# Optimization experiments

Hardware: AMD Instinct MI355X
Metric: run time of the kernel (lower is better)

Reference implementation:

```python
import jax, jax.numpy as jnp
import numpy as np

H, LMAX, NSEG, EPS = 8, 2, 16, 1e-7
S = (LMAX + 1) ** 2  # 9 spherical components
L_OF_M = jnp.asarray(np.floor(np.sqrt(np.arange(S))).astype(np.int32))  # degree l of each m-component


def so3_linear(x, W, b):
    # x [n,S,Cin]; W [LMAX+1,Cin,Cout] per-degree weights; bias only on l=0 (invariant) component
    y = jnp.einsum('nsi,sio->nso', x, W[L_OF_M])
    return y + b[None, None, :] * (jnp.arange(S) == 0)[None, :, None]


def equiv_layernorm(x, gamma, beta):
    # x [N,S,C]; standard LN on l=0 scalars, RMS-of-irrep-norm scaling (equivariant) for l>0
    x0 = x[:, 0, :]
    mu = jnp.mean(x0, -1, keepdims=True)
    var = jnp.mean((x0 - mu) ** 2, -1, keepdims=True)
    outs = [(((x0 - mu) / jnp.sqrt(var + EPS)) * gamma[0] + beta)[:, None, :]]
    for l in range(1, LMAX + 1):
        xl = x[:, l * l:(l + 1) * (l + 1), :]               # [N,2l+1,C]
        n2 = jnp.mean(xl * xl, axis=1)                      # [N,C] mean sq over m
        rms = jnp.sqrt(jnp.mean(n2, -1, keepdims=True) + EPS)  # [N,1]
        outs.append(xl / rms[:, None, :] * gamma[l][None, None, :])
    return jnp.concatenate(outs, axis=1)


def setup_inputs() -> dict:
    key = jax.random.key(0)
    ks = jax.random.split(key, 12)
    N, E, CIN, CH = 512, 8192, 128, 256
    return dict(
        q=jax.random.normal(ks[0], (N, S, CIN), jnp.float32),
        k=jax.random.normal(ks[1], (N, S, CIN), jnp.float32),
        v=jax.random.normal(ks[2], (N, S, CIN), jnp.float32),
        envelope=jax.random.uniform(ks[3], (E,), jnp.float32),
        attn_bias=jax.random.normal(ks[4], (H, E), jnp.float32),
        atom_index=jax.random.randint(ks[5], (E,), 0, N),
        batch_index=jnp.sort(jax.random.randint(ks[6], (E,), 0, NSEG)),
        edge_map_tab=jax.random.randint(ks[7], (E,), 0, E),
        Wq=jax.random.normal(ks[8], (LMAX + 1, CIN, CH), jnp.float32) / np.float32(np.sqrt(CIN)),
        bq=jnp.zeros((CH,), jnp.float32),
        Wk=jax.random.normal(ks[9], (LMAX + 1, CIN, CH), jnp.float32) / np.float32(np.sqrt(CIN)),
        bk=jnp.zeros((CH,), jnp.float32),
        Wv=jax.random.normal(ks[10], (LMAX + 1, CIN, CH), jnp.float32) / np.float32(np.sqrt(CIN)),
        bv=jnp.zeros((CH,), jnp.float32),
        gamma=jnp.ones((LMAX + 1, CH), jnp.float32),
        beta=jnp.zeros((CH,), jnp.float32),
        Wo=jax.random.normal(ks[11], (LMAX + 1, CH, CIN), jnp.float32) / np.float32(np.sqrt(CH)),
        bo=jnp.zeros((CIN,), jnp.float32),
    )


def reference(q, k, v, envelope, attn_bias, atom_index, batch_index, edge_map_tab,
              Wq, bq, Wk, bk, Wv, bv, gamma, beta, Wo, bo):
    N, E = q.shape[0], atom_index.shape[0]
    qh = so3_linear(q, Wq, bq)                      # [N,S,CH]
    kh = so3_linear(k, Wk, bk)[atom_index]          # [E,S,CH] gather per edge
    vh = so3_linear(v, Wv, bv)[atom_index]
    CH = qh.shape[-1]
    d = CH // H
    qh = qh.reshape(N, S, H, d).transpose(2, 0, 1, 3).reshape(H, N, S * d)
    kh = kh.reshape(E, S, H, d).transpose(2, 0, 1, 3).reshape(H, E, S * d)
    vh = vh.reshape(E, S, H, d).transpose(2, 0, 1, 3).reshape(H, E, S * d)
    scale = np.float32(np.sqrt(d / 3.0) / d)
    scores = jnp.einsum('hnf,hef->hne', qh * scale, kh)         # [H,N,E]
    scores = scores + attn_bias[:, edge_map_tab][:, None, :]
    env_e = envelope[edge_map_tab]                               # [E]
    # smooth scatter softmax grouped by batch_index over edge axis
    st = scores.transpose(2, 0, 1)                               # [E,H,N]
    mx = jax.ops.segment_max(st, batch_index, num_segments=NSEG)
    rec = jnp.exp(st - mx[batch_index]) * env_e[:, None, None]
    den = jax.ops.segment_sum(rec, batch_index, num_segments=NSEG)
    attn = rec / (den[batch_index] + 1e-16)
    attn = (attn * env_e[:, None, None]).transpose(1, 2, 0)      # [H,N,E]
    out = jnp.einsum('hne,hef->hnf', attn, vh)                   # [H,N,S*d]
    out = out.transpose(1, 0, 2).reshape(N, H, S, d).transpose(0, 2, 1, 3).reshape(N, S, CH)
    out = equiv_layernorm(out, gamma, beta)
    return so3_linear(out, Wo, bo)
```

## Files before the change

### kernel.cpp

```cpp
#include <hip/hip_runtime.h>
#include <hip/hip_bf16.h>
#include <math.h>

#define NH 8
#define SDIM 9
#define NSEG 16
#define NATOM 512
#define NEDGE 8192
#define CIN 128
#define CHN 256
#define DH 32
#define FDIM 288
#define EPS 1e-7f
#define SCALE 0.10206207261596577f

typedef __attribute__((ext_vector_type(8))) short bf16x8;
typedef __attribute__((ext_vector_type(8))) short short8;
typedef __attribute__((ext_vector_type(4))) float f32x4;

__device__ inline float blockReduceMax(float v, float* red) {
    #pragma unroll
    for (int off = 32; off; off >>= 1) v = fmaxf(v, __shfl_xor(v, off, 64));
    int lane = threadIdx.x & 63, wid = threadIdx.x >> 6;
    if (lane == 0) red[wid] = v;
    __syncthreads();
    v = fmaxf(fmaxf(red[0], red[1]), fmaxf(red[2], red[3]));
    __syncthreads();
    return v;
}
__device__ inline int lower_bound_batch(const int* __restrict__ b, int val) {
    int lo = 0, hi = NEDGE;
    while (lo < hi) {
        int mid = (lo + hi) >> 1;
        if (b[mid] < val) lo = mid + 1; else hi = mid;
    }
    return lo;
}
__device__ inline ushort f2bu(float x) {
    __hip_bfloat16 b = __float2bfloat16(x);
    return *(ushort*)&b;
}

__global__ void __launch_bounds__(256) wtrans(const float* __restrict__ Wq, const float* __restrict__ Wk,
                                              const float* __restrict__ Wv, const float* __restrict__ Wo,
                                              ushort* __restrict__ WqT, ushort* __restrict__ WkT,
                                              ushort* __restrict__ WvT, ushort* __restrict__ WoT) {
    const int bid = blockIdx.x;
    const int tid = threadIdx.x;
    __shared__ float tile[64][33];
    const float* src; ushort* dst; int R, C, r0, c0;
    if (bid < 144) {
        const int z = bid / 48;
        const int rem = bid % 48;
        const int l = rem >> 4;
        const int t = rem & 15;
        R = CIN; C = CHN;
        r0 = (t >> 3) * 64; c0 = (t & 7) * 32;
        src = ((z == 0) ? Wq : (z == 1) ? Wk : Wv) + (size_t)l * R * C;
        dst = ((z == 0) ? WqT : (z == 1) ? WkT : WvT) + (size_t)l * R * C;
    } else {
        const int rem = bid - 144;
        const int l = rem >> 4;
        const int t = rem & 15;
        R = CHN; C = CIN;
        r0 = (t >> 2) * 64; c0 = (t & 3) * 32;
        src = Wo + (size_t)l * R * C;
        dst = WoT + (size_t)l * R * C;
    }
    #pragma unroll
    for (int p = 0; p < 8; ++p) {
        int row = p * 8 + (tid >> 5);
        int col = tid & 31;
        tile[row][col] = src[(size_t)(r0 + row) * C + c0 + col];
    }
    __syncthreads();
    #pragma unroll
    for (int p = 0; p < 8; ++p) {
        int c = p * 4 + (tid >> 6);
        int rr = tid & 63;
        dst[(size_t)(c0 + c) * R + r0 + rr] = f2bu(tile[rr][c]);
    }
}

__global__ void __launch_bounds__(256) stage1(const int* __restrict__ batch,
                                              const int* __restrict__ am, const int* __restrict__ emap,
                                              const float* __restrict__ envelope,
                                              const float* __restrict__ attn_bias,
                                              float* __restrict__ E1, float* __restrict__ E2,
                                              const float* __restrict__ q, const float* __restrict__ k,
                                              const float* __restrict__ v,
                                              const ushort* __restrict__ WqT, const ushort* __restrict__ WkT,
                                              const ushort* __restrict__ WvT,
                                              const float* __restrict__ bq, const float* __restrict__ bk,
                                              const float* __restrict__ bv,
                                              ushort* __restrict__ qhB,
                                              ushort* __restrict__ khB,
                                              ushort* __restrict__ vhT,
                                              float* __restrict__ stats) {
    const int bid = blockIdx.x;
    const int tid = threadIdx.x;
    if (bid < NSEG * NH) {
        const int seg = bid & (NSEG - 1), h = bid >> 4;
        __shared__ float e1[NATOM];
        __shared__ float e2[NATOM];
        __shared__ float red[4];
        e1[tid] = 0.f; e1[tid + 256] = 0.f;
        e2[tid] = 0.f; e2[tid + 256] = 0.f;
        const float* bh = attn_bias + (size_t)h * NEDGE;
        float mv = -1e30f;
        for (int e = tid; e < NEDGE; e += 256) mv = fmaxf(mv, bh[e]);
        const float mb = blockReduceMax(mv, red);
        const int st = lower_bound_batch(batch, seg);
        const int en = lower_bound_batch(batch, seg + 1);
        for (int e = st + tid; e < en; e += 256) {
            int m = am[e], em = emap[e];
            float ev = envelope[em];
            float eb = __expf(bh[em] - mb);
            atomicAdd(&e1[m], ev * eb);
            atomicAdd(&e2[m], ev * ev * eb);
        }
        __syncthreads();
        size_t base = ((size_t)h * NSEG + seg) * NATOM;
        E1[base + tid] = e1[tid]; E1[base + tid + 256] = e1[tid + 256];
        E2[base + tid] = e2[tid]; E2[base + tid + 256] = e2[tid + 256];
        return;
    }
    if (bid < NSEG * NH + 432) {
        const int idx = bid - NSEG * NH;
        const int z = idx / 144;
        const int rem = idx - z * 144;
        const int s = rem >> 4;
        const int n0 = (rem & 15) * 32;
        const int l = (s == 0) ? 0 : ((s < 4) ? 1 : 2);
        const float* x = (z == 0) ? q : (z == 1) ? k : v;
        const ushort* WT = ((z == 0) ? WqT : (z == 1) ? WkT : WvT) + (size_t)l * CIN * CHN;
        const float* bias = (z == 0) ? bq : (z == 1) ? bk : bv;
        const int lane = tid & 63, w = tid >> 6;
        const int wr = w >> 1, wc = w & 1;
        const int r = lane & 15, kg = lane >> 4;
        const int arow = n0 + 16 * wr + r;
        const float* xrow = x + ((size_t)arow * SDIM + s) * CIN;
        f32x4 acc[8] = {};
        #pragma unroll
        for (int ks = 0; ks < 4; ++ks) {
            const int k0 = ks * 32 + kg * 8;
            float4 x0 = *(const float4*)(xrow + k0);
            float4 x1 = *(const float4*)(xrow + k0 + 4);
            bf16x8 a;
            a[0] = f2bu(x0.x); a[1] = f2bu(x0.y); a[2] = f2bu(x0.z); a[3] = f2bu(x0.w);
            a[4] = f2bu(x1.x); a[5] = f2bu(x1.y); a[6] = f2bu(x1.z); a[7] = f2bu(x1.w);
            #pragma unroll
            for (int j = 0; j < 8; ++j) {
                const int o = 128 * wc + 16 * j + r;
                bf16x8 bf = *(const bf16x8*)(WT + (size_t)o * CIN + k0);
                acc[j] = __builtin_amdgcn_mfma_f32_16x16x32_bf16(a, bf, acc[j], 0, 0, 0);
            }
        }
        const float sc = (z == 0) ? SCALE : 1.0f;
        #pragma unroll
        for (int j = 0; j < 8; ++j) {
            const int o = 128 * wc + 16 * j + r;
            const float bb = (s == 0) ? bias[o] : 0.f;
            const int h = o >> 5, dj = o & 31;
            const int f = s * DH + dj;
            if (z < 2) {
                ushort* dst = (z == 0) ? qhB : khB;
                #pragma unroll
                for (int p = 0; p < 4; ++p) {
                    int row = n0 + 16 * wr + kg * 4 + p;
                    dst[((size_t)h * NATOM + row) * FDIM + f] = f2bu((acc[j][p] + bb) * sc);
                }
            } else {
                ushort* dst = vhT + ((size_t)h * FDIM + f) * NATOM;
                #pragma unroll
                for (int p = 0; p < 4; ++p) {
                    int row = n0 + 16 * wr + kg * 4 + p;
                    dst[row] = f2bu(acc[j][p] + bb);
                }
            }
        }
        return;
    }
    {
        float4 z4 = {0.f, 0.f, 0.f, 0.f};
        float4* sp = (float4*)stats;
        sp[tid] = z4;
        sp[tid + 256] = z4;
    }
}

#define SBST 520
__global__ void __launch_bounds__(256) attn_out_fused(const ushort* __restrict__ qhB,
                                                      const ushort* __restrict__ khB,
                                                      const ushort* __restrict__ vhT,
                                                      const float* __restrict__ E1,
                                                      const float* __restrict__ E2,
                                                      float* __restrict__ attnOut,
                                                      float* __restrict__ stats) {
    const int h = blockIdx.y;
    const int n0 = blockIdx.x * 16;
    __shared__ float E1s[NSEG][NATOM];
    __shared__ float E2s[NSEG][NATOM];
    __shared__ float rowmax[4][16];
    __shared__ float Dpart[4][16][NSEG];
    __shared__ float invDs[16][NSEG];
    const int tid = threadIdx.x;
    const int lane = tid & 63, w = tid >> 6;
    const int r = lane & 15, kg = lane >> 4;
    {
        const float* e1g = E1 + (size_t)h * NSEG * NATOM;
        const float* e2g = E2 + (size_t)h * NSEG * NATOM;
        for (int i = tid * 4; i < NSEG * NATOM; i += 1024) {
            *(float4*)&((float*)E1s)[i] = *(const float4*)&e1g[i];
            *(float4*)&((float*)E2s)[i] = *(const float4*)&e2g[i];
        }
    }
    const ushort* A = qhB + (size_t)h * NATOM * FDIM;
    const ushort* B = khB + (size_t)h * NATOM * FDIM;
    const int ar = n0 + r;
    f32x4 acc[8] = {};
    #pragma unroll
    for (int ks = 0; ks < FDIM / 32; ++ks) {
        const int k0 = ks * 32 + kg * 8;
        bf16x8 a = *(const bf16x8*)(A + (size_t)ar * FDIM + k0);
        #pragma unroll
        for (int j = 0; j < 8; ++j) {
            const int bcol = w * 128 + 16 * j + r;
            bf16x8 b = *(const bf16x8*)(B + (size_t)bcol * FDIM + k0);
            acc[j] = __builtin_amdgcn_mfma_f32_16x16x32_bf16(a, b, acc[j], 0, 0, 0);
        }
    }
    __syncthreads();
    float pm[4];
    #pragma unroll
    for (int p = 0; p < 4; ++p) {
        float m = acc[0][p];
        #pragma unroll
        for (int j = 1; j < 8; ++j) m = fmaxf(m, acc[j][p]);
        pm[p] = m;
    }
    #pragma unroll
    for (int mk = 1; mk < 16; mk <<= 1)
        #pragma unroll
        for (int p = 0; p < 4; ++p) pm[p] = fmaxf(pm[p], __shfl_xor(pm[p], mk, 64));
    if (r == 0) {
        #pragma unroll
        for (int p = 0; p < 4; ++p) rowmax[w][kg * 4 + p] = pm[p];
    }
    __syncthreads();
    float mx[4];
    #pragma unroll
    for (int p = 0; p < 4; ++p) {
        int row = kg * 4 + p;
        mx[p] = fmaxf(fmaxf(rowmax[0][row], rowmax[1][row]),
                      fmaxf(rowmax[2][row], rowmax[3][row]));
    }
    float es[8][4];
    #pragma unroll
    for (int j = 0; j < 8; ++j)
        #pragma unroll
        for (int p = 0; p < 4; ++p) es[j][p] = __expf(acc[j][p] - mx[p]);
    float Dp[4][NSEG] = {};
    #pragma unroll
    for (int j = 0; j < 8; ++j) {
        const int col = w * 128 + 16 * j + r;
        #pragma unroll
        for (int g = 0; g < NSEG; ++g) {
            float e1 = E1s[g][col];
            #pragma unroll
            for (int p = 0; p < 4; ++p) Dp[p][g] += es[j][p] * e1;
        }
    }
    #pragma unroll
    for (int mk = 1; mk < 16; mk <<= 1)
        #pragma unroll
        for (int p = 0; p < 4; ++p)
            #pragma unroll
            for (int g = 0; g < NSEG; ++g) Dp[p][g] += __shfl_xor(Dp[p][g], mk, 64);
    if (r == 0) {
        #pragma unroll
        for (int p = 0; p < 4; ++p)
            #pragma unroll
            for (int g = 0; g < NSEG; ++g) Dpart[w][kg * 4 + p][g] = Dp[p][g];
    }
    __syncthreads();
    {
        int row = tid >> 4, g = tid & 15;
        float d = Dpart[0][row][g] + Dpart[1][row][g] + Dpart[2][row][g] + Dpart[3][row][g];
        invDs[row][g] = 1.0f / (d + 1e-30f);
    }
    __syncthreads();
    float iv[4][NSEG];
    #pragma unroll
    for (int p = 0; p < 4; ++p)
        #pragma unroll
        for (int g = 0; g < NSEG; ++g) iv[p][g] = invDs[kg * 4 + p][g];
    ushort* sbuf = (ushort*)E1s;
    #pragma unroll
    for (int j = 0; j < 8; ++j) {
        const int col = w * 128 + 16 * j + r;
        float ww[4] = {};
        #pragma unroll
        for (int g = 0; g < NSEG; ++g) {
            float e2 = E2s[g][col];
            #pragma unroll
            for (int p = 0; p < 4; ++p) ww[p] += e2 * iv[p][g];
        }
        #pragma unroll
        for (int p = 0; p < 4; ++p)
            sbuf[(kg * 4 + p) * SBST + col] = f2bu(es[j][p] * ww[p]);
    }
    __syncthreads();
    const ushort* Bv = vhT + (size_t)h * FDIM * NATOM;
    float S0[4] = {}, Q0[4] = {}, Q1[4] = {}, Q2[4] = {};
    for (int fc = w; fc < FDIM / 16; fc += 4) {
        const int f0 = fc * 16;
        f32x4 oacc = {};
        #pragma unroll
        for (int ks = 0; ks < NATOM / 32; ++ks) {
            const int k0 = ks * 32 + kg * 8;
            bf16x8 a = *(const bf16x8*)(sbuf + r * SBST + k0);
            bf16x8 b = *(const bf16x8*)(Bv + (size_t)(f0 + r) * NATOM + k0);
            oacc = __builtin_amdgcn_mfma_f32_16x16x32_bf16(a, b, oacc, 0, 0, 0);
        }
        const int f = f0 + r;
        const int s = f >> 5, dj = f & 31;
        #pragma unroll
        for (int p = 0; p < 4; ++p) {
            const int row = n0 + kg * 4 + p;
            float x = oacc[p];
            attnOut[((size_t)row * SDIM + s) * CHN + h * DH + dj] = x;
            if (s == 0) { S0[p] += x; Q0[p] += x * x; }
            else if (s < 4) Q1[p] += x * x;
            else Q2[p] += x * x;
        }
    }
    #pragma unroll
    for (int mk = 1; mk < 16; mk <<= 1)
        #pragma unroll
        for (int p = 0; p < 4; ++p) {
            S0[p] += __shfl_xor(S0[p], mk, 64);
            Q0[p] += __shfl_xor(Q0[p], mk, 64);
            Q1[p] += __shfl_xor(Q1[p], mk, 64);
            Q2[p] += __shfl_xor(Q2[p], mk, 64);
        }
    if (r == 0) {
        #pragma unroll
        for (int p = 0; p < 4; ++p) {
            const int row = n0 + kg * 4 + p;
            atomicAdd(&stats[row * 4 + 0], S0[p]);
            atomicAdd(&stats[row * 4 + 1], Q0[p]);
            atomicAdd(&stats[row * 4 + 2], Q1[p]);
            atomicAdd(&stats[row * 4 + 3], Q2[p]);
        }
    }
}

__global__ void __launch_bounds__(256) so3out_ln(const float* __restrict__ attnOut,
                                                 const float* __restrict__ stats,
                                                 const float* __restrict__ gamma,
                                                 const float* __restrict__ beta,
                                                 const ushort* __restrict__ WoT,
                                                 const float* __restrict__ bo,
                                                 float* __restrict__ out) {
    const int s = blockIdx.y;
    const int n0 = blockIdx.x * 16;
    const int l = (s == 0) ? 0 : ((s < 4) ? 1 : 2);
    const int tid = threadIdx.x;
    const int lane = tid & 63, w = tid >> 6;
    const int r = lane & 15, kg = lane >> 4;
    const int ar = n0 + r;
    float mu, ivl;
    {
        float s0 = stats[ar * 4 + 0];
        float q0 = stats[ar * 4 + 1];
        float q1 = stats[ar * 4 + 2];
        float q2 = stats[ar * 4 + 3];
        float m0 = s0 * (1.0f / CHN);
        float var = q0 * (1.0f / CHN) - m0 * m0;
        if (s == 0) { mu = m0; ivl = 1.0f / sqrtf(var + EPS); }
        else if (s < 4) { mu = 0.f; ivl = 1.0f / sqrtf(q1 * (1.0f / (3 * CHN)) + EPS); }
        else { mu = 0.f; ivl = 1.0f / sqrtf(q2 * (1.0f / (5 * CHN)) + EPS); }
    }
    const float* xrow = attnOut + ((size_t)ar * SDIM + s) * CHN;
    const float* gl = gamma + l * CHN;
    const ushort* B = WoT + (size_t)l * CIN * CHN;
    f32x4 acc[2] = {};
    #pragma unroll
    for (int ks = 0; ks < CHN / 32; ++ks) {
        const int k0 = ks * 32 + kg * 8;
        float4 x0 = *(const float4*)(xrow + k0);
        float4 x1 = *(const float4*)(xrow + k0 + 4);
        float4 g0 = *(const float4*)(gl + k0);
        float4 g1 = *(const float4*)(gl + k0 + 4);
        float y[8];
        y[0] = (x0.x - mu) * ivl * g0.x; y[1] = (x0.y - mu) * ivl * g0.y;
        y[2] = (x0.z - mu) * ivl * g0.z; y[3] = (x0.w - mu) * ivl * g0.w;
        y[4] = (x1.x - mu) * ivl * g1.x; y[5] = (x1.y - mu) * ivl * g1.y;
        y[6] = (x1.z - mu) * ivl * g1.z; y[7] = (x1.w - mu) * ivl * g1.w;
        if (s == 0) {
            float4 b0 = *(const float4*)(beta + k0);
            float4 b1 = *(const float4*)(beta + k0 + 4);
            y[0] += b0.x; y[1] += b0.y; y[2] += b0.z; y[3] += b0.w;
            y[4] += b1.x; y[5] += b1.y; y[6] += b1.z; y[7] += b1.w;
        }
        bf16x8 a;
        #pragma unroll
        for (int jj = 0; jj < 8; ++jj) a[jj] = f2bu(y[jj]);
        bf16x8 b0f = *(const bf16x8*)(B + (size_t)(32 * w + 16 * 0 + r) * CHN + k0);
        bf16x8 b1f = *(const bf16x8*)(B + (size_t)(32 * w + 16 * 1 + r) * CHN + k0);
        acc[0] = __builtin_amdgcn_mfma_f32_16x16x32_bf16(a, b0f, acc[0], 0, 0, 0);
        acc[1] = __builtin_amdgcn_mfma_f32_16x16x32_bf16(a, b1f, acc[1], 0, 0, 0);
    }
    #pragma unroll
    for (int j = 0; j < 2; ++j) {
        const int o = 32 * w + 16 * j + r;
        const float badd = (s == 0) ? bo[o] : 0.f;
        #pragma unroll
        for (int p = 0; p < 4; ++p) {
            const int n = n0 + kg * 4 + p;
            out[((size_t)n * SDIM + s) * CIN + o] = acc[j][p] + badd;
        }
    }
}

extern "C" void kernel_launch(void* const* d_in, const int* in_sizes, int n_in,
                              void* d_out, int out_size, void* d_ws, size_t ws_size,
                              hipStream_t stream) {
    const float* q = (const float*)d_in[0];
    const float* k = (const float*)d_in[1];
    const float* v = (const float*)d_in[2];
    const float* envelope = (const float*)d_in[3];
    const float* attn_bias = (const float*)d_in[4];
    const int* atom_index = (const int*)d_in[5];
    const int* batch_index = (const int*)d_in[6];
    const int* edge_map = (const int*)d_in[7];
    const float* Wq = (const float*)d_in[8];
    const float* bq = (const float*)d_in[9];
    const float* Wk = (const float*)d_in[10];
    const float* bk = (const float*)d_in[11];
    const float* Wv = (const float*)d_in[12];
    const float* bv = (const float*)d_in[13];
    const float* gamma = (const float*)d_in[14];
    const float* beta = (const float*)d_in[15];
    const float* Wo = (const float*)d_in[16];
    const float* bo = (const float*)d_in[17];
    float* out = (float*)d_out;

    const size_t SZ_HNF = (size_t)NH * NATOM * FDIM;
    const size_t SZ_TAB = (size_t)NH * NSEG * NATOM;
    const size_t SZ_WOT = (size_t)3 * CIN * CHN;
    const size_t SZ_NSC = (size_t)NATOM * SDIM * CHN;

    char* wsb = (char*)d_ws;
    ushort* qhB = (ushort*)wsb;
    ushort* khB = qhB + SZ_HNF;
    ushort* vhT = khB + SZ_HNF;
    float* attnOut = (float*)(vhT + SZ_HNF);
    float* E1 = attnOut + SZ_NSC;
    float* E2 = E1 + SZ_TAB;
    ushort* WqT = (ushort*)(E2 + SZ_TAB);
    ushort* WkT = WqT + SZ_WOT;
    ushort* WvT = WkT + SZ_WOT;
    ushort* WoT = WvT + SZ_WOT;
    float* stats = (float*)(WoT + SZ_WOT);

    size_t needed = 2 * 3 * SZ_HNF + 4 * SZ_NSC + 4 * 2 * SZ_TAB
                  + 2 * 4 * SZ_WOT + 4 * NATOM * 4 + 256;
    if (ws_size < needed) return;

    wtrans<<<192, 256, 0, stream>>>(Wq, Wk, Wv, Wo, WqT, WkT, WvT, WoT);
    stage1<<<NSEG * NH + 432 + 1, 256, 0, stream>>>(
        batch_index, atom_index, edge_map, envelope, attn_bias, E1, E2,
        q, k, v, WqT, WkT, WvT, bq, bk, bv, qhB, khB, vhT, stats);
    attn_out_fused<<<dim3(NATOM / 16, NH), 256, 0, stream>>>(
        qhB, khB, vhT, E1, E2, attnOut, stats);
    so3out_ln<<<dim3(NATOM / 16, SDIM), 256, 0, stream>>>(
        attnOut, stats, gamma, beta, WoT, bo, out);
}
```

Baseline: 86.80 us.

## Split fused attention into softmax kernel and separate attn-V GEMM kernel

```diff
diff --git a/kernel.cpp b/kernel.cpp
--- a/kernel.cpp
+++ b/kernel.cpp
@@ -190,53 +190,41 @@
 }
 
 #define SBST 520
-__global__ void __launch_bounds__(256) attn_out_fused(const ushort* __restrict__ qhB,
-                                                      const ushort* __restrict__ khB,
-                                                      const ushort* __restrict__ vhT,
-                                                      const float* __restrict__ E1,
-                                                      const float* __restrict__ E2,
-                                                      float* __restrict__ attnOut,
-                                                      float* __restrict__ stats) {
+__global__ void __launch_bounds__(512) attn_fused(const ushort* __restrict__ qhB,
+                                                  const ushort* __restrict__ khB,
+                                                  const float* __restrict__ E1,
+                                                  const float* __restrict__ E2,
+                                                  ushort* __restrict__ attnB) {
     const int h = blockIdx.y;
     const int n0 = blockIdx.x * 16;
-    __shared__ float E1s[NSEG][NATOM];
-    __shared__ float E2s[NSEG][NATOM];
-    __shared__ float rowmax[4][16];
-    __shared__ float Dpart[4][16][NSEG];
+    __shared__ ushort sbuf[16 * SBST];
+    __shared__ float rowmax[8][16];
+    __shared__ float Dpart[8][16][NSEG];
     __shared__ float invDs[16][NSEG];
     const int tid = threadIdx.x;
     const int lane = tid & 63, w = tid >> 6;
     const int r = lane & 15, kg = lane >> 4;
-    {
-        const float* e1g = E1 + (size_t)h * NSEG * NATOM;
-        const float* e2g = E2 + (size_t)h * NSEG * NATOM;
-        for (int i = tid * 4; i < NSEG * NATOM; i += 1024) {
-            *(float4*)&((float*)E1s)[i] = *(const float4*)&e1g[i];
-            *(float4*)&((float*)E2s)[i] = *(const float4*)&e2g[i];
-        }
-    }
     const ushort* A = qhB + (size_t)h * NATOM * FDIM;
     const ushort* B = khB + (size_t)h * NATOM * FDIM;
+    const float* e1g = E1 + (size_t)h * NSEG * NATOM;
+    const float* e2g = E2 + (size_t)h * NSEG * NATOM;
     const int ar = n0 + r;
-    f32x4 acc[8] = {};
+    f32x4 acc[4] = {};
     #pragma unroll
     for (int ks = 0; ks < FDIM / 32; ++ks) {
         const int k0 = ks * 32 + kg * 8;
         bf16x8 a = *(const bf16x8*)(A + (size_t)ar * FDIM + k0);
         #pragma unroll
-        for (int j = 0; j < 8; ++j) {
-            const int bcol = w * 128 + 16 * j + r;
+        for (int j = 0; j < 4; ++j) {
+            const int bcol = w * 64 + 16 * j + r;
             bf16x8 b = *(const bf16x8*)(B + (size_t)bcol * FDIM + k0);
             acc[j] = __builtin_amdgcn_mfma_f32_16x16x32_bf16(a, b, acc[j], 0, 0, 0);
         }
     }
-    __syncthreads();
     float pm[4];
     #pragma unroll
     for (int p = 0; p < 4; ++p) {
-        float m = acc[0][p];
-        #pragma unroll
-        for (int j = 1; j < 8; ++j) m = fmaxf(m, acc[j][p]);
+        float m = fmaxf(fmaxf(acc[0][p], acc[1][p]), fmaxf(acc[2][p], acc[3][p]));
         pm[p] = m;
     }
     #pragma unroll
@@ -251,22 +239,24 @@
     float mx[4];
     #pragma unroll
     for (int p = 0; p < 4; ++p) {
-        int row = kg * 4 + p;
-        mx[p] = fmaxf(fmaxf(rowmax[0][row], rowmax[1][row]),
-                      fmaxf(rowmax[2][row], rowmax[3][row]));
-    }
-    float es[8][4];
-    #pragma unroll
-    for (int j = 0; j < 8; ++j)
+        const int row = kg * 4 + p;
+        float m = rowmax[0][row];
+        #pragma unroll
+        for (int ww2 = 1; ww2 < 8; ++ww2) m = fmaxf(m, rowmax[ww2][row]);
+        mx[p] = m;
+    }
+    float es[4][4];
+    #pragma unroll
+    for (int j = 0; j < 4; ++j)
         #pragma unroll
         for (int p = 0; p < 4; ++p) es[j][p] = __expf(acc[j][p] - mx[p]);
     float Dp[4][NSEG] = {};
     #pragma unroll
-    for (int j = 0; j < 8; ++j) {
-        const int col = w * 128 + 16 * j + r;
+    for (int j = 0; j < 4; ++j) {
+        const int col = w * 64 + 16 * j + r;
         #pragma unroll
         for (int g = 0; g < NSEG; ++g) {
-            float e1 = E1s[g][col];
+            float e1 = e1g[(size_t)g * NATOM + col];
             #pragma unroll
             for (int p = 0; p < 4; ++p) Dp[p][g] += es[j][p] * e1;
         }
@@ -284,9 +274,11 @@
             for (int g = 0; g < NSEG; ++g) Dpart[w][kg * 4 + p][g] = Dp[p][g];
     }
     __syncthreads();
-    {
-        int row = tid >> 4, g = tid & 15;
-        float d = Dpart[0][row][g] + Dpart[1][row][g] + Dpart[2][row][g] + Dpart[3][row][g];
+    if (tid < 256) {
+        const int row = tid >> 4, g = tid & 15;
+        float d = 0.f;
+        #pragma unroll
+        for (int ww2 = 0; ww2 < 8; ++ww2) d += Dpart[ww2][row][g];
         invDs[row][g] = 1.0f / (d + 1e-30f);
     }
     __syncthreads();
@@ -295,14 +287,13 @@
     for (int p = 0; p < 4; ++p)
         #pragma unroll
         for (int g = 0; g < NSEG; ++g) iv[p][g] = invDs[kg * 4 + p][g];
-    ushort* sbuf = (ushort*)E1s;
-    #pragma unroll
-    for (int j = 0; j < 8; ++j) {
-        const int col = w * 128 + 16 * j + r;
+    #pragma unroll
+    for (int j = 0; j < 4; ++j) {
+        const int col = w * 64 + 16 * j + r;
         float ww[4] = {};
         #pragma unroll
         for (int g = 0; g < NSEG; ++g) {
-            float e2 = E2s[g][col];
+            float e2 = e2g[(size_t)g * NATOM + col];
             #pragma unroll
             for (int p = 0; p < 4; ++p) ww[p] += e2 * iv[p][g];
         }
@@ -311,47 +302,73 @@
             sbuf[(kg * 4 + p) * SBST + col] = f2bu(es[j][p] * ww[p]);
     }
     __syncthreads();
-    const ushort* Bv = vhT + (size_t)h * FDIM * NATOM;
-    float S0[4] = {}, Q0[4] = {}, Q1[4] = {}, Q2[4] = {};
-    for (int fc = w; fc < FDIM / 16; fc += 4) {
-        const int f0 = fc * 16;
-        f32x4 oacc = {};
-        #pragma unroll
-        for (int ks = 0; ks < NATOM / 32; ++ks) {
-            const int k0 = ks * 32 + kg * 8;
-            bf16x8 a = *(const bf16x8*)(sbuf + r * SBST + k0);
-            bf16x8 b = *(const bf16x8*)(Bv + (size_t)(f0 + r) * NATOM + k0);
-            oacc = __builtin_amdgcn_mfma_f32_16x16x32_bf16(a, b, oacc, 0, 0, 0);
-        }
-        const int f = f0 + r;
-        const int s = f >> 5, dj = f & 31;
+    {
+        ushort* dst = attnB + ((size_t)h * NATOM + n0) * NATOM;
+        #pragma unroll
+        for (int i = tid * 8; i < 16 * NATOM; i += 4096) {
+            const int row = i >> 9, col = i & 511;
+            *(short8*)(dst + (size_t)row * NATOM + col) = *(short8*)(sbuf + row * SBST + col);
+        }
+    }
+}
+
+__global__ void __launch_bounds__(256) gemm_out_stats(const ushort* __restrict__ attnB,
+                                                      const ushort* __restrict__ vhT,
+                                                      float* __restrict__ attnOut,
+                                                      float* __restrict__ stats) {
+    const int h = blockIdx.z;
+    const int fb = blockIdx.x;
+    const int n0 = blockIdx.y * 64;
+    const int tid = threadIdx.x;
+    const int lane = tid & 63, w = tid >> 6;
+    const int r = lane & 15, kg = lane >> 4;
+    const ushort* A = attnB + (size_t)h * NATOM * NATOM;
+    const ushort* B = vhT + (size_t)h * FDIM * NATOM;
+    const int ar = n0 + 16 * w + r;
+    f32x4 acc[2] = {};
+    #pragma unroll 4
+    for (int ks = 0; ks < NATOM / 32; ++ks) {
+        const int k0 = ks * 32 + kg * 8;
+        bf16x8 a = *(const bf16x8*)(A + (size_t)ar * NATOM + k0);
+        bf16x8 b0 = *(const bf16x8*)(B + (size_t)(32 * fb + r) * NATOM + k0);
+        bf16x8 b1 = *(const bf16x8*)(B + (size_t)(32 * fb + 16 + r) * NATOM + k0);
+        acc[0] = __builtin_amdgcn_mfma_f32_16x16x32_bf16(a, b0, acc[0], 0, 0, 0);
+        acc[1] = __builtin_amdgcn_mfma_f32_16x16x32_bf16(a, b1, acc[1], 0, 0, 0);
+    }
+    float sA[4], sB[4];
+    #pragma unroll
+    for (int p = 0; p < 4; ++p) { sA[p] = 0.f; sB[p] = 0.f; }
+    #pragma unroll
+    for (int j = 0; j < 2; ++j) {
+        const int dj = 16 * j + r;
         #pragma unroll
         for (int p = 0; p < 4; ++p) {
-            const int row = n0 + kg * 4 + p;
-            float x = oacc[p];
-            attnOut[((size_t)row * SDIM + s) * CHN + h * DH + dj] = x;
-            if (s == 0) { S0[p] += x; Q0[p] += x * x; }
-            else if (s < 4) Q1[p] += x * x;
-            else Q2[p] += x * x;
+            const int row = n0 + 16 * w + kg * 4 + p;
+            float x = acc[j][p];
+            attnOut[((size_t)row * SDIM + fb) * CHN + h * DH + dj] = x;
+            sA[p] += x;
+            sB[p] += x * x;
         }
     }
     #pragma unroll
     for (int mk = 1; mk < 16; mk <<= 1)
         #pragma unroll
         for (int p = 0; p < 4; ++p) {
-            S0[p] += __shfl_xor(S0[p], mk, 64);
-            Q0[p] += __shfl_xor(Q0[p], mk, 64);
-            Q1[p] += __shfl_xor(Q1[p], mk, 64);
-            Q2[p] += __shfl_xor(Q2[p], mk, 64);
+            sA[p] += __shfl_xor(sA[p], mk, 64);
+            sB[p] += __shfl_xor(sB[p], mk, 64);
         }
     if (r == 0) {
         #pragma unroll
         for (int p = 0; p < 4; ++p) {
-            const int row = n0 + kg * 4 + p;
-            atomicAdd(&stats[row * 4 + 0], S0[p]);
-            atomicAdd(&stats[row * 4 + 1], Q0[p]);
-            atomicAdd(&stats[row * 4 + 2], Q1[p]);
-            atomicAdd(&stats[row * 4 + 3], Q2[p]);
+            const int row = n0 + 16 * w + kg * 4 + p;
+            if (fb == 0) {
+                atomicAdd(&stats[row * 4 + 0], sA[p]);
+                atomicAdd(&stats[row * 4 + 1], sB[p]);
+            } else if (fb < 4) {
+                atomicAdd(&stats[row * 4 + 2], sB[p]);
+            } else {
+                atomicAdd(&stats[row * 4 + 3], sB[p]);
+            }
         }
     }
 }
@@ -407,8 +424,8 @@
         bf16x8 a;
         #pragma unroll
         for (int jj = 0; jj < 8; ++jj) a[jj] = f2bu(y[jj]);
-        bf16x8 b0f = *(const bf16x8*)(B + (size_t)(32 * w + 16 * 0 + r) * CHN + k0);
-        bf16x8 b1f = *(const bf16x8*)(B + (size_t)(32 * w + 16 * 1 + r) * CHN + k0);
+        bf16x8 b0f = *(const bf16x8*)(B + (size_t)(32 * w + r) * CHN + k0);
+        bf16x8 b1f = *(const bf16x8*)(B + (size_t)(32 * w + 16 + r) * CHN + k0);
         acc[0] = __builtin_amdgcn_mfma_f32_16x16x32_bf16(a, b0f, acc[0], 0, 0, 0);
         acc[1] = __builtin_amdgcn_mfma_f32_16x16x32_bf16(a, b1f, acc[1], 0, 0, 0);
     }
@@ -448,6 +465,7 @@
     float* out = (float*)d_out;
 
     const size_t SZ_HNF = (size_t)NH * NATOM * FDIM;
+    const size_t SZ_HNN = (size_t)NH * NATOM * NATOM;
     const size_t SZ_TAB = (size_t)NH * NSEG * NATOM;
     const size_t SZ_WOT = (size_t)3 * CIN * CHN;
     const size_t SZ_NSC = (size_t)NATOM * SDIM * CHN;
@@ -456,7 +474,8 @@
     ushort* qhB = (ushort*)wsb;
     ushort* khB = qhB + SZ_HNF;
     ushort* vhT = khB + SZ_HNF;
-    float* attnOut = (float*)(vhT + SZ_HNF);
+    ushort* attnB = vhT + SZ_HNF;
+    float* attnOut = (float*)(attnB + SZ_HNN);
     float* E1 = attnOut + SZ_NSC;
     float* E2 = E1 + SZ_TAB;
     ushort* WqT = (ushort*)(E2 + SZ_TAB);
@@ -465,7 +484,7 @@
     ushort* WoT = WvT + SZ_WOT;
     float* stats = (float*)(WoT + SZ_WOT);
 
-    size_t needed = 2 * 3 * SZ_HNF + 4 * SZ_NSC + 4 * 2 * SZ_TAB
+    size_t needed = 2 * 3 * SZ_HNF + 2 * SZ_HNN + 4 * SZ_NSC + 4 * 2 * SZ_TAB
                   + 2 * 4 * SZ_WOT + 4 * NATOM * 4 + 256;
     if (ws_size < needed) return;
 
@@ -473,8 +492,7 @@
     stage1<<<NSEG * NH + 432 + 1, 256, 0, stream>>>(
         batch_index, atom_index, edge_map, envelope, attn_bias, E1, E2,
         q, k, v, WqT, WkT, WvT, bq, bk, bv, qhB, khB, vhT, stats);
-    attn_out_fused<<<dim3(NATOM / 16, NH), 256, 0, stream>>>(
-        qhB, khB, vhT, E1, E2, attnOut, stats);
-    so3out_ln<<<dim3(NATOM / 16, SDIM), 256, 0, stream>>>(
-        attnOut, stats, gamma, beta, WoT, bo, out);
-}
+    attn_fused<<<dim3(NATOM / 16, NH), 512, 0, stream>>>(qhB, khB, E1, E2, attnB);
+    gemm_out_stats<<<dim3(SDIM, NATOM / 64, NH), 256, 0, stream>>>(attnB, vhT, attnOut, stats);
+    so3out_ln<<<dim3(NATOM / 16, SDIM), 256, 0, stream>>>(attnOut, stats, gamma, beta, WoT, bo, out);
+}
```

Result: faster. 79.92 us (-7.9%).

## Double attention block to 512 threads and read envelope tables from global

Applied to the files above, without the earlier changes.

```diff
diff --git a/kernel.cpp b/kernel.cpp
--- a/kernel.cpp
+++ b/kernel.cpp
@@ -190,7 +190,7 @@
 }
 
 #define SBST 520
-__global__ void __launch_bounds__(256) attn_out_fused(const ushort* __restrict__ qhB,
+__global__ void __launch_bounds__(512) attn_out_fused(const ushort* __restrict__ qhB,
                                                       const ushort* __restrict__ khB,
                                                       const ushort* __restrict__ vhT,
                                                       const float* __restrict__ E1,
@@ -199,46 +199,34 @@
                                                       float* __restrict__ stats) {
     const int h = blockIdx.y;
     const int n0 = blockIdx.x * 16;
-    __shared__ float E1s[NSEG][NATOM];
-    __shared__ float E2s[NSEG][NATOM];
-    __shared__ float rowmax[4][16];
-    __shared__ float Dpart[4][16][NSEG];
+    __shared__ ushort sbuf[16 * SBST];
+    __shared__ float rowmax[8][16];
+    __shared__ float Dpart[8][16][NSEG];
     __shared__ float invDs[16][NSEG];
     const int tid = threadIdx.x;
     const int lane = tid & 63, w = tid >> 6;
     const int r = lane & 15, kg = lane >> 4;
-    {
-        const float* e1g = E1 + (size_t)h * NSEG * NATOM;
-        const float* e2g = E2 + (size_t)h * NSEG * NATOM;
-        for (int i = tid * 4; i < NSEG * NATOM; i += 1024) {
-            *(float4*)&((float*)E1s)[i] = *(const float4*)&e1g[i];
-            *(float4*)&((float*)E2s)[i] = *(const float4*)&e2g[i];
-        }
-    }
     const ushort* A = qhB + (size_t)h * NATOM * FDIM;
     const ushort* B = khB + (size_t)h * NATOM * FDIM;
+    const float* e1g = E1 + (size_t)h * NSEG * NATOM;
+    const float* e2g = E2 + (size_t)h * NSEG * NATOM;
     const int ar = n0 + r;
-    f32x4 acc[8] = {};
+    f32x4 acc[4] = {};
     #pragma unroll
     for (int ks = 0; ks < FDIM / 32; ++ks) {
         const int k0 = ks * 32 + kg * 8;
         bf16x8 a = *(const bf16x8*)(A + (size_t)ar * FDIM + k0);
         #pragma unroll
-        for (int j = 0; j < 8; ++j) {
-            const int bcol = w * 128 + 16 * j + r;
+        for (int j = 0; j < 4; ++j) {
+            const int bcol = w * 64 + 16 * j + r;
             bf16x8 b = *(const bf16x8*)(B + (size_t)bcol * FDIM + k0);
             acc[j] = __builtin_amdgcn_mfma_f32_16x16x32_bf16(a, b, acc[j], 0, 0, 0);
         }
     }
-    __syncthreads();
     float pm[4];
     #pragma unroll
-    for (int p = 0; p < 4; ++p) {
-        float m = acc[0][p];
-        #pragma unroll
-        for (int j = 1; j < 8; ++j) m = fmaxf(m, acc[j][p]);
-        pm[p] = m;
-    }
+    for (int p = 0; p < 4; ++p)
+        pm[p] = fmaxf(fmaxf(acc[0][p], acc[1][p]), fmaxf(acc[2][p], acc[3][p]));
     #pragma unroll
     for (int mk = 1; mk < 16; mk <<= 1)
         #pragma unroll
@@ -251,22 +239,24 @@
     float mx[4];
     #pragma unroll
     for (int p = 0; p < 4; ++p) {
-        int row = kg * 4 + p;
-        mx[p] = fmaxf(fmaxf(rowmax[0][row], rowmax[1][row]),
-                      fmaxf(rowmax[2][row], rowmax[3][row]));
-    }
-    float es[8][4];
-    #pragma unroll
-    for (int j = 0; j < 8; ++j)
+        const int row = kg * 4 + p;
+        float m = rowmax[0][row];
+        #pragma unroll
+        for (int ww2 = 1; ww2 < 8; ++ww2) m = fmaxf(m, rowmax[ww2][row]);
+        mx[p] = m;
+    }
+    float es[4][4];
+    #pragma unroll
+    for (int j = 0; j < 4; ++j)
         #pragma unroll
         for (int p = 0; p < 4; ++p) es[j][p] = __expf(acc[j][p] - mx[p]);
     float Dp[4][NSEG] = {};
     #pragma unroll
-    for (int j = 0; j < 8; ++j) {
-        const int col = w * 128 + 16 * j + r;
+    for (int j = 0; j < 4; ++j) {
+        const int col = w * 64 + 16 * j + r;
         #pragma unroll
         for (int g = 0; g < NSEG; ++g) {
-            float e1 = E1s[g][col];
+            float e1 = e1g[(size_t)g * NATOM + col];
             #pragma unroll
             for (int p = 0; p < 4; ++p) Dp[p][g] += es[j][p] * e1;
         }
@@ -284,9 +274,11 @@
             for (int g = 0; g < NSEG; ++g) Dpart[w][kg * 4 + p][g] = Dp[p][g];
     }
     __syncthreads();
-    {
-        int row = tid >> 4, g = tid & 15;
-        float d = Dpart[0][row][g] + Dpart[1][row][g] + Dpart[2][row][g] + Dpart[3][row][g];
+    if (tid < 256) {
+        const int row = tid >> 4, g = tid & 15;
+        float d = 0.f;
+        #pragma unroll
+        for (int ww2 = 0; ww2 < 8; ++ww2) d += Dpart[ww2][row][g];
         invDs[row][g] = 1.0f / (d + 1e-30f);
     }
     __syncthreads();
@@ -295,14 +287,13 @@
     for (int p = 0; p < 4; ++p)
         #pragma unroll
         for (int g = 0; g < NSEG; ++g) iv[p][g] = invDs[kg * 4 + p][g];
-    ushort* sbuf = (ushort*)E1s;
-    #pragma unroll
-    for (int j = 0; j < 8; ++j) {
-        const int col = w * 128 + 16 * j + r;
+    #pragma unroll
+    for (int j = 0; j < 4; ++j) {
+        const int col = w * 64 + 16 * j + r;
         float ww[4] = {};
         #pragma unroll
         for (int g = 0; g < NSEG; ++g) {
-            float e2 = E2s[g][col];
+            float e2 = e2g[(size_t)g * NATOM + col];
             #pragma unroll
             for (int p = 0; p < 4; ++p) ww[p] += e2 * iv[p][g];
         }
@@ -313,8 +304,8 @@
     __syncthreads();
     const ushort* Bv = vhT + (size_t)h * FDIM * NATOM;
     float S0[4] = {}, Q0[4] = {}, Q1[4] = {}, Q2[4] = {};
-    for (int fc = w; fc < FDIM / 16; fc += 4) {
-        const int f0 = fc * 16;
+    for (int fi = w; fi < FDIM / 16; fi += 8) {
+        const int f0 = fi * 16;
         f32x4 oacc = {};
         #pragma unroll
         for (int ks = 0; ks < NATOM / 32; ++ks) {
@@ -407,8 +398,8 @@
         bf16x8 a;
         #pragma unroll
         for (int jj = 0; jj < 8; ++jj) a[jj] = f2bu(y[jj]);
-        bf16x8 b0f = *(const bf16x8*)(B + (size_t)(32 * w + 16 * 0 + r) * CHN + k0);
-        bf16x8 b1f = *(const bf16x8*)(B + (size_t)(32 * w + 16 * 1 + r) * CHN + k0);
+        bf16x8 b0f = *(const bf16x8*)(B + (size_t)(32 * w + r) * CHN + k0);
+        bf16x8 b1f = *(const bf16x8*)(B + (size_t)(32 * w + 16 + r) * CHN + k0);
         acc[0] = __builtin_amdgcn_mfma_f32_16x16x32_bf16(a, b0f, acc[0], 0, 0, 0);
         acc[1] = __builtin_amdgcn_mfma_f32_16x16x32_bf16(a, b1f, acc[1], 0, 0, 0);
     }
@@ -473,7 +464,7 @@
     stage1<<<NSEG * NH + 432 + 1, 256, 0, stream>>>(
         batch_index, atom_index, edge_map, envelope, attn_bias, E1, E2,
         q, k, v, WqT, WkT, WvT, bq, bk, bv, qhB, khB, vhT, stats);
-    attn_out_fused<<<dim3(NATOM / 16, NH), 256, 0, stream>>>(
+    attn_out_fused<<<dim3(NATOM / 16, NH), 512, 0, stream>>>(
         qhB, khB, vhT, E1, E2, attnOut, stats);
     so3out_ln<<<dim3(NATOM / 16, SDIM), 256, 0, stream>>>(
         attnOut, stats, gamma, beta, WoT, bo, out);
```

Result: slower. 99.81 us (+15.0%).
